# Performance work log

Hardware: AMD Instinct MI355X
Metric: run time of the kernel (lower is better)

Reference implementation:

```python
import jax, jax.numpy as jnp
import numpy as np

NUM_TEAMS = 200000
EMBED_DIM = 16
NUM_EDGES = 3200000
BATCH = 500000
EPS_NORM = 1e-12  # F.normalize clamp
EPS_SOFTMAX = 1e-16  # PyG edge-softmax denom eps
NEG_SLOPE = 0.01  # LeakyReLU default


def setup_inputs() -> dict:
    key = jax.random.key(0)
    ks = jax.random.split(key, 12)
    inp = {}
    inp["embed"] = jax.random.normal(ks[0], (NUM_TEAMS, EMBED_DIM), dtype=jnp.float32)
    inp["beta"] = jnp.ones((2,), dtype=jnp.float32)  # one learnable scalar per AGNNConv
    # torch Linear init ~ U(-1/sqrt(fan_in), 1/sqrt(fan_in)); stored as [in, out]
    def lin(k, fi, fo):
        b = 1.0 / np.sqrt(fi)
        k1, k2 = jax.random.split(k)
        return (jax.random.uniform(k1, (fi, fo), jnp.float32, -b, b),
                jax.random.uniform(k2, (fo,), jnp.float32, -b, b))
    inp["lin0_w"], inp["lin0_b"] = lin(ks[1], 2 * EMBED_DIM, 6)
    inp["lin1_w"], inp["lin1_b"] = lin(ks[2], 6, 16)
    inp["lin2_w"], inp["lin2_b"] = lin(ks[3], 16, 3)
    inp["edge_index"] = jax.random.randint(ks[4], (2, NUM_EDGES), 0, NUM_TEAMS, dtype=jnp.int64)
    inp["home"] = jax.random.randint(ks[5], (BATCH,), 0, NUM_TEAMS, dtype=jnp.int64)
    inp["away"] = jax.random.randint(ks[6], (BATCH,), 0, NUM_TEAMS, dtype=jnp.int64)
    return inp


def _agnn_conv(x, beta, src, dst, n):
    # x: [N, D]; messages flow src(j) -> dst(i); scatter-softmax over edges per dst
    xn = x / jnp.maximum(jnp.linalg.norm(x, axis=-1, keepdims=True), EPS_NORM)
    alpha = beta * jnp.sum(xn[src] * xn[dst], axis=-1)          # [E]
    m = jax.ops.segment_max(alpha, dst, num_segments=n)          # [N]
    a = jnp.exp(alpha - m[dst])                                   # [E]
    denom = jax.ops.segment_sum(a, dst, num_segments=n)          # [N]
    a = a / (denom[dst] + EPS_SOFTMAX)
    return jax.ops.segment_sum(a[:, None] * x[src], dst, num_segments=n)  # [N, D]


def _forward(embed, beta, lin0_w, lin0_b, lin1_w, lin1_b, lin2_w, lin2_b,
             src, dst, home, away):
    n = embed.shape[0]
    act = lambda v: jax.nn.leaky_relu(v, NEG_SLOPE)
    x = embed  # embedding of arange(n_teams) == the table itself
    x = act(_agnn_conv(x, beta[0], src, dst, n))
    x = act(_agnn_conv(x, beta[1], src, dst, n))
    h = jnp.concatenate([x[home], x[away]], axis=-1)  # [B, 2D]
    h = act(h @ lin0_w + lin0_b)
    h = act(h @ lin1_w + lin1_b)
    h = act(h @ lin2_w + lin2_b)
    return jax.nn.log_softmax(h, axis=0).reshape(-1, 3)  # LogSoftmax(dim=0), faithful


def reference(embed, beta, lin0_w, lin0_b, lin1_w, lin1_b, lin2_w, lin2_b,
              edge_index, home, away):
    n = embed.shape[0]
    # AGNNConv default: remove then add self-loops
    loops = jnp.arange(n, dtype=edge_index.dtype)
    mask = edge_index[0] != edge_index[1]
    safe = jnp.where(mask, edge_index[1], edge_index[0])  # self-loop-out non-loop edges
    src = jnp.concatenate([edge_index[0], loops])
    dst = jnp.concatenate([jnp.where(mask, edge_index[1], edge_index[0]), loops])
    # masked self-loops in original list become src==dst duplicates of the appended
    # self-loops only if random collision; to faithfully *remove* them we redirect
    # removed edges onto the node's own appended self-loop (alpha identical for
    # src==dst), which changes only duplicate self-loop counts with prob ~1/N.
    return _forward(embed, beta, lin0_w, lin0_b, lin1_w, lin1_b, lin2_w, lin2_b,
                    src, dst, home, away)
```

## Files before the change

kernel.cpp:

```cpp
#include <hip/hip_runtime.h>
#include <hip/hip_fp16.h>
#include <math.h>

#define TPB 256
#define NPB 512
#define NPB_SHIFT 9
#define EPB 8192
#define EPW 16
#define BCAP 12288
#define RSTRIDE 32

typedef float v2f __attribute__((ext_vector_type(2)));

__device__ __forceinline__ float leaky_relu(float v) { return v > 0.0f ? v : 0.01f * v; }

__device__ __forceinline__ float dot4(float4 a, float4 b) {
    return a.x * b.x + a.y * b.y + a.z * b.z + a.w * b.w;
}
__device__ __forceinline__ float4 f4_scale(float4 a, float s) {
    return make_float4(a.x * s, a.y * s, a.z * s, a.w * s);
}
__device__ __forceinline__ float4 f4_acc(float4 a, float w, float4 y) {
    return make_float4(fmaf(w, y.x, a.x), fmaf(w, y.y, a.y),
                       fmaf(w, y.z, a.z), fmaf(w, y.w, a.w));
}
__device__ __forceinline__ float4 f4_add_shfl(float4 v, int d) {
    return make_float4(v.x + __shfl_xor(v.x, d, 64), v.y + __shfl_xor(v.y, d, 64),
                       v.z + __shfl_xor(v.z, d, 64), v.w + __shfl_xor(v.w, d, 64));
}
__device__ __forceinline__ float4 leaky4(float4 v) {
    return make_float4(leaky_relu(v.x), leaky_relu(v.y), leaky_relu(v.z), leaky_relu(v.w));
}

__device__ __forceinline__ float4 dec4(unsigned w) {
    v2f lo = __builtin_amdgcn_cvt_pk_f32_fp8((int)w, false);
    v2f hi = __builtin_amdgcn_cvt_pk_f32_fp8((int)w, true);
    return make_float4(lo.x, lo.y, hi.x, hi.y);
}
__device__ __forceinline__ unsigned enc4(float4 v) {
    int r = __builtin_amdgcn_cvt_pk_fp8_f32(v.x, v.y, 0, false);
    r = __builtin_amdgcn_cvt_pk_fp8_f32(v.z, v.w, r, true);
    return (unsigned)r;
}

__device__ __forceinline__ void store_h4(__half* row, int l, float4 v) {
    union { float2 f; __half h[4]; } u;
    u.h[0] = __float2half(v.x); u.h[1] = __float2half(v.y);
    u.h[2] = __float2half(v.z); u.h[3] = __float2half(v.w);
    ((float2*)row)[l] = u.f;
}

__device__ __forceinline__ uint4 rec_q(const char* base, int i) {
    return *(const uint4*)(base + (size_t)i * RSTRIDE);
}
__device__ __forceinline__ float rec_n(const char* base, int i) {
    return *(const float*)(base + (size_t)i * RSTRIDE + 16);
}

__device__ __forceinline__ int wave_incl_scan(int v, int lane) {
#pragma unroll
    for (int off = 1; off < 64; off <<= 1) {
        int u = __shfl_up(v, off, 64);
        if (lane >= off) v += u;
    }
    return v;
}

__global__ void k_binA(const int* __restrict__ src, const int* __restrict__ dst,
                       unsigned* __restrict__ bdata, int* __restrict__ cbase,
                       int* __restrict__ ccnt, int E, int K,
                       const float* __restrict__ x, char* __restrict__ xqn,
                       int N) {
    __shared__ int hist[512];
    __shared__ unsigned lcol[EPB];
    __shared__ int wsum[8];
    int t = threadIdx.x;
    int lane = t & 63, wv = t >> 6;
    int c = blockIdx.x;
    int e0 = c * EPB;
    int e1 = min(e0 + EPB, E);
    int tot = e1 - e0;
    hist[t] = 0;
    __syncthreads();
    int myd[EPW], mys[EPW];
    if (tot == EPB) {
        const int4* d4 = (const int4*)(dst + e0);
        const int4* s4 = (const int4*)(src + e0);
#pragma unroll
        for (int k = 0; k < 4; ++k) {
            int4 dd = d4[t + k * 512];
            int4 ss = s4[t + k * 512];
            myd[4 * k + 0] = dd.x; myd[4 * k + 1] = dd.y;
            myd[4 * k + 2] = dd.z; myd[4 * k + 3] = dd.w;
            mys[4 * k + 0] = ss.x; mys[4 * k + 1] = ss.y;
            mys[4 * k + 2] = ss.z; mys[4 * k + 3] = ss.w;
            atomicAdd(&hist[dd.x >> NPB_SHIFT], 1);
            atomicAdd(&hist[dd.y >> NPB_SHIFT], 1);
            atomicAdd(&hist[dd.z >> NPB_SHIFT], 1);
            atomicAdd(&hist[dd.w >> NPB_SHIFT], 1);
        }
    } else {
#pragma unroll
        for (int k = 0; k < EPW; ++k) {
            int e = e0 + t + k * 512;
            int d = (e < e1) ? dst[e] : -1;
            mys[k] = (e < e1) ? src[e] : 0;
            myd[k] = d;
            if (d >= 0) atomicAdd(&hist[d >> NPB_SHIFT], 1);
        }
    }
    __syncthreads();
    int v = hist[t];
    int inc = wave_incl_scan(v, lane);
    if (lane == 63) wsum[wv] = inc;
    __syncthreads();
    if (t == 0) {
        int acc = 0;
#pragma unroll
        for (int k = 0; k < 8; ++k) { int xv = wsum[k]; wsum[k] = acc; acc += xv; }
    }
    __syncthreads();
    int excl = inc + wsum[wv] - v;
    if (t < K) {
        cbase[(size_t)c * K + t] = excl;
        ccnt[(size_t)c * K + t] = v;
    }
    __syncthreads();
    hist[t] = excl;
    __syncthreads();
    if (tot == EPB) {
#pragma unroll
        for (int k = 0; k < EPW; ++k) {
            int d = myd[k];
            int p = atomicAdd(&hist[d >> NPB_SHIFT], 1);
            lcol[p] = ((unsigned)(d & (NPB - 1)) << 18) | (unsigned)mys[k];
        }
    } else {
#pragma unroll
        for (int k = 0; k < EPW; ++k) {
            int d = myd[k];
            if (d >= 0) {
                int p = atomicAdd(&hist[d >> NPB_SHIFT], 1);
                lcol[p] = ((unsigned)(d & (NPB - 1)) << 18) | (unsigned)mys[k];
            }
        }
    }
    __syncthreads();
    unsigned* outp = bdata + (size_t)c * EPB;
    for (int i = t; i < tot; i += 512) outp[i] = lcol[i];
    int i = c * 512 + t;
    if (i < N) {
        const float4* xp = (const float4*)(x + (size_t)i * 16);
        float4 a = xp[0], b = xp[1], cc = xp[2], d = xp[3];
        float ss = dot4(a, a) + dot4(b, b) + dot4(cc, cc) + dot4(d, d);
        float nn = fmaxf(sqrtf(ss), 1e-12f);
        float inv = 1.0f / nn;
        char* rp = xqn + (size_t)i * RSTRIDE;
        *(uint4*)rp = make_uint4(enc4(f4_scale(a, inv)), enc4(f4_scale(b, inv)),
                                 enc4(f4_scale(cc, inv)), enc4(f4_scale(d, inv)));
        *(float*)(rp + 16) = nn;
    }
}

__global__ void k_binB(const unsigned* __restrict__ bdata, const int* __restrict__ cbase,
                       const int* __restrict__ ccnt,
                       int* __restrict__ startp, int* __restrict__ endp,
                       int* __restrict__ col, int N, int NC, int K) {
    __shared__ int cb[512];
    __shared__ int cc[512];
    __shared__ int ldeg[NPB];
    __shared__ int wsum[8];
    int b = blockIdx.x, t = threadIdx.x;
    int lane = t & 63, wv = t >> 6;
    int n0 = b << NPB_SHIFT;
    int nn = min(NPB, N - n0);
    cb[t] = (t < NC) ? cbase[(size_t)t * K + b] : 0;
    cc[t] = (t < NC) ? ccnt[(size_t)t * K + b] : 0;
    ldeg[t] = 0;
    __syncthreads();
    int mycnt = (t < NC) ? cc[t] : 0;
    const unsigned* myp = bdata + (size_t)t * EPB + cb[t];
    for (int k = 0; k < mycnt; ++k) {
        unsigned e = myp[k];
        atomicAdd(&ldeg[e >> 18], 1);
    }
    __syncthreads();
    int dv = ldeg[t];
    int inc = wave_incl_scan(dv, lane);
    if (lane == 63) wsum[wv] = inc;
    __syncthreads();
    if (t == 0) {
        int acc = 0;
#pragma unroll
        for (int k = 0; k < 8; ++k) { int xv = wsum[k]; wsum[k] = acc; acc += xv; }
    }
    __syncthreads();
    int excl = inc + wsum[wv] - dv;
    int gb = b * BCAP;
    if (t < nn) {
        startp[n0 + t] = gb + excl;
        endp[n0 + t] = gb + excl + dv;
    }
    __syncthreads();
    ldeg[t] = excl;
    __syncthreads();
    for (int k = 0; k < mycnt; ++k) {
        unsigned e = myp[k];
        int pos = atomicAdd(&ldeg[e >> 18], 1);
        col[gb + pos] = (int)(e & 0x3FFFFu);
    }
}

__global__ void k_agnn(const char* __restrict__ xqn,
                       const int* __restrict__ startp, const int* __restrict__ endp,
                       const int* __restrict__ col,
                       const float* __restrict__ beta_ptr, int beta_idx,
                       void* __restrict__ out, int n, int fp8_out) {
    int t = threadIdx.x;
    int l = t & 7;
    int i = blockIdx.x * (512 / 8) + (t >> 3);
    if (i >= n) return;
    float bet = beta_ptr[beta_idx];
    uint4 rowi = rec_q(xqn, i);
    float ni = rec_n(xqn, i);
    float4 x0 = dec4(rowi.x), x1 = dec4(rowi.y), x2 = dec4(rowi.z), x3 = dec4(rowi.w);
    float4 q0 = f4_scale(x0, bet), q1 = f4_scale(x1, bet),
           q2 = f4_scale(x2, bet), q3 = f4_scale(x3, bet);
    float s;
    float4 a0, a1, a2, a3;
    if (l == 0) {
        float aself = dot4(x0, q0) + dot4(x1, q1) + dot4(x2, q2) + dot4(x3, q3);
        float w = __expf(aself);
        s = w;
        float wi = w * ni;
        a0 = f4_scale(x0, wi); a1 = f4_scale(x1, wi);
        a2 = f4_scale(x2, wi); a3 = f4_scale(x3, wi);
    } else {
        s = 0.0f;
        a0 = a1 = a2 = a3 = make_float4(0.f, 0.f, 0.f, 0.f);
    }
    int e1 = endp[i];
    int last = max(e1 - 1, 0);
    int e = startp[i] + l;
    int j0 = min(max(col[min(e, last)], 0), n - 1);
    uint4 rA = rec_q(xqn, j0);
    float nA = rec_n(xqn, j0);
    int j1 = min(max(col[min(e + 8, last)], 0), n - 1);
    uint4 rB = rec_q(xqn, j1);
    float nB = rec_n(xqn, j1);
    for (; e < e1; e += 8) {
        int j2 = min(max(col[min(e + 16, last)], 0), n - 1);
        uint4 rC = rec_q(xqn, j2);
        float nC = rec_n(xqn, j2);
        float4 y0 = dec4(rA.x), y1 = dec4(rA.y), y2 = dec4(rA.z), y3 = dec4(rA.w);
        float d = dot4(y0, q0) + dot4(y1, q1) + dot4(y2, q2) + dot4(y3, q3);
        float w = __expf(d);
        s += w;
        float wn = w * nA;
        a0 = f4_acc(a0, wn, y0);
        a1 = f4_acc(a1, wn, y1);
        a2 = f4_acc(a2, wn, y2);
        a3 = f4_acc(a3, wn, y3);
        rA = rB; nA = nB; rB = rC; nB = nC;
    }
#pragma unroll
    for (int d_ = 1; d_ < 8; d_ <<= 1) {
        s += __shfl_xor(s, d_, 64);
        a0 = f4_add_shfl(a0, d_);
        a1 = f4_add_shfl(a1, d_);
        a2 = f4_add_shfl(a2, d_);
        a3 = f4_add_shfl(a3, d_);
    }
    float inv = 1.0f / (s + 1e-16f);
    float4 o0 = leaky4(f4_scale(a0, inv));
    float4 o1 = leaky4(f4_scale(a1, inv));
    float4 o2 = leaky4(f4_scale(a2, inv));
    float4 o3 = leaky4(f4_scale(a3, inv));
    if (l < 4) {
        float4 oq = (l == 0) ? o0 : (l == 1) ? o1 : (l == 2) ? o2 : o3;
        if (fp8_out) {
            float ss = dot4(o0, o0) + dot4(o1, o1) + dot4(o2, o2) + dot4(o3, o3);
            float nn = fmaxf(sqrtf(ss), 1e-12f);
            char* rp = (char*)out + (size_t)i * RSTRIDE;
            ((unsigned*)rp)[l] = enc4(f4_scale(oq, 1.0f / nn));
            if (l == 0) *(float*)(rp + 16) = nn;
        } else {
            store_h4((__half*)out + (size_t)i * 16, l, oq);
        }
    }
}

__global__ void k_mlp(const __half* __restrict__ x, const int* __restrict__ home,
                      const int* __restrict__ away,
                      const float* __restrict__ w0, const float* __restrict__ b0,
                      const float* __restrict__ w1, const float* __restrict__ b1,
                      const float* __restrict__ w2, const float* __restrict__ b2,
                      float* __restrict__ z, float* __restrict__ bmax,
                      float* __restrict__ bsum, int nb) {
    __shared__ float sw0[192], sw1[96], sw2[48], sb0[6], sb1[16], sb2[3];
    __shared__ float rmax[4][3];
    __shared__ float rsum[4][3];
    int t = threadIdx.x;
    if (t < 192) sw0[t] = w0[t];
    if (t < 96)  sw1[t] = w1[t];
    if (t < 48)  sw2[t] = w2[t];
    if (t < 6)   sb0[t] = b0[t];
    if (t < 16)  sb1[t] = b1[t];
    if (t < 3)   sb2[t] = b2[t];
    __syncthreads();
    int i = blockIdx.x * blockDim.x + t;
    bool act = i < nb;
    float z0 = -3.4e38f, z1 = -3.4e38f, z2 = -3.4e38f;
    if (act) {
        float h[32];
        const uint4* hr = (const uint4*)(x + (size_t)home[i] * 16);
        const uint4* ar = (const uint4*)(x + (size_t)away[i] * 16);
        uint4 hv0 = hr[0], hv1 = hr[1];
        uint4 av0 = ar[0], av1 = ar[1];
        union { uint4 u; __half2 h2[4]; } cv;
#pragma unroll
        for (int q = 0; q < 4; ++q) {
            cv.u = (q == 0) ? hv0 : (q == 1) ? hv1 : (q == 2) ? av0 : av1;
#pragma unroll
            for (int k = 0; k < 4; ++k) {
                float2 f = __half22float2(cv.h2[k]);
                h[q * 8 + 2 * k + 0] = f.x;
                h[q * 8 + 2 * k + 1] = f.y;
            }
        }
        float t0[6];
#pragma unroll
        for (int o = 0; o < 6; ++o) {
            float acc = sb0[o];
#pragma unroll
            for (int k = 0; k < 32; ++k) acc = fmaf(h[k], sw0[k * 6 + o], acc);
            t0[o] = leaky_relu(acc);
        }
        float t1[16];
#pragma unroll
        for (int o = 0; o < 16; ++o) {
            float acc = sb1[o];
#pragma unroll
            for (int k = 0; k < 6; ++k) acc = fmaf(t0[k], sw1[k * 16 + o], acc);
            t1[o] = leaky_relu(acc);
        }
        float zz[3];
#pragma unroll
        for (int o = 0; o < 3; ++o) {
            float acc = sb2[o];
#pragma unroll
            for (int k = 0; k < 16; ++k) acc = fmaf(t1[k], sw2[k * 3 + o], acc);
            zz[o] = leaky_relu(acc);
            z[(size_t)i * 3 + o] = zz[o];
        }
        z0 = zz[0]; z1 = zz[1]; z2 = zz[2];
    }
    float w0_ = z0, w1_ = z1, w2_ = z2;
#pragma unroll
    for (int off = 32; off > 0; off >>= 1) {
        w0_ = fmaxf(w0_, __shfl_down(w0_, off));
        w1_ = fmaxf(w1_, __shfl_down(w1_, off));
        w2_ = fmaxf(w2_, __shfl_down(w2_, off));
    }
    int wid = t >> 6;
    if ((t & 63) == 0) { rmax[wid][0] = w0_; rmax[wid][1] = w1_; rmax[wid][2] = w2_; }
    __syncthreads();
    float M0 = fmaxf(fmaxf(rmax[0][0], rmax[1][0]), fmaxf(rmax[2][0], rmax[3][0]));
    float M1 = fmaxf(fmaxf(rmax[0][1], rmax[1][1]), fmaxf(rmax[2][1], rmax[3][1]));
    float M2 = fmaxf(fmaxf(rmax[0][2], rmax[1][2]), fmaxf(rmax[2][2], rmax[3][2]));
    float e0 = act ? __expf(z0 - M0) : 0.0f;
    float e1 = act ? __expf(z1 - M1) : 0.0f;
    float e2 = act ? __expf(z2 - M2) : 0.0f;
#pragma unroll
    for (int off = 32; off > 0; off >>= 1) {
        e0 += __shfl_down(e0, off);
        e1 += __shfl_down(e1, off);
        e2 += __shfl_down(e2, off);
    }
    if ((t & 63) == 0) { rsum[wid][0] = e0; rsum[wid][1] = e1; rsum[wid][2] = e2; }
    __syncthreads();
    if (t == 0) {
        float S0 = rsum[0][0] + rsum[1][0] + rsum[2][0] + rsum[3][0];
        float S1 = rsum[0][1] + rsum[1][1] + rsum[2][1] + rsum[3][1];
        float S2 = rsum[0][2] + rsum[1][2] + rsum[2][2] + rsum[3][2];
        bmax[blockIdx.x * 3 + 0] = M0; bmax[blockIdx.x * 3 + 1] = M1; bmax[blockIdx.x * 3 + 2] = M2;
        bsum[blockIdx.x * 3 + 0] = S0; bsum[blockIdx.x * 3 + 1] = S1; bsum[blockIdx.x * 3 + 2] = S2;
    }
}

__global__ void k_lse(const float* __restrict__ bmax, const float* __restrict__ bsum,
                      float* __restrict__ gM, float* __restrict__ gS, int nblk) {
    __shared__ float lm[4][3];
    __shared__ float ls[4][3];
    int t = threadIdx.x;
    float M0 = -3.4e38f, M1 = -3.4e38f, M2 = -3.4e38f;
    float S0 = 0.f, S1 = 0.f, S2 = 0.f;
    for (int b = t; b < nblk; b += 256) {
        float m0 = bmax[b * 3 + 0], s0 = bsum[b * 3 + 0];
        float n0 = fmaxf(M0, m0); S0 = S0 * __expf(M0 - n0) + s0 * __expf(m0 - n0); M0 = n0;
        float m1 = bmax[b * 3 + 1], s1 = bsum[b * 3 + 1];
        float n1 = fmaxf(M1, m1); S1 = S1 * __expf(M1 - n1) + s1 * __expf(m1 - n1); M1 = n1;
        float m2 = bmax[b * 3 + 2], s2 = bsum[b * 3 + 2];
        float n2 = fmaxf(M2, m2); S2 = S2 * __expf(M2 - n2) + s2 * __expf(m2 - n2); M2 = n2;
    }
#pragma unroll
    for (int off = 32; off > 0; off >>= 1) {
        float mo, so, nm;
        mo = __shfl_down(M0, off); so = __shfl_down(S0, off);
        nm = fmaxf(M0, mo); S0 = S0 * __expf(M0 - nm) + so * __expf(mo - nm); M0 = nm;
        mo = __shfl_down(M1, off); so = __shfl_down(S1, off);
        nm = fmaxf(M1, mo); S1 = S1 * __expf(M1 - nm) + so * __expf(mo - nm); M1 = nm;
        mo = __shfl_down(M2, off); so = __shfl_down(S2, off);
        nm = fmaxf(M2, mo); S2 = S2 * __expf(M2 - nm) + so * __expf(mo - nm); M2 = nm;
    }
    int wid = t >> 6;
    if ((t & 63) == 0) {
        lm[wid][0] = M0; lm[wid][1] = M1; lm[wid][2] = M2;
        ls[wid][0] = S0; ls[wid][1] = S1; ls[wid][2] = S2;
    }
    __syncthreads();
    if (t == 0) {
        for (int w = 1; w < 4; ++w) {
            float nm;
            nm = fmaxf(M0, lm[w][0]); S0 = S0 * __expf(M0 - nm) + ls[w][0] * __expf(lm[w][0] - nm); M0 = nm;
            nm = fmaxf(M1, lm[w][1]); S1 = S1 * __expf(M1 - nm) + ls[w][1] * __expf(lm[w][1] - nm); M1 = nm;
            nm = fmaxf(M2, lm[w][2]); S2 = S2 * __expf(M2 - nm) + ls[w][2] * __expf(lm[w][2] - nm); M2 = nm;
        }
        gM[0] = M0; gM[1] = M1; gM[2] = M2;
        gS[0] = S0; gS[1] = S1; gS[2] = S2;
    }
}

__device__ __forceinline__ float pick3(int c, float L0, float L1, float L2) {
    return c == 0 ? L0 : (c == 1 ? L1 : L2);
}

__global__ void k_final(const float4* __restrict__ z4, const float* __restrict__ gM,
                        const float* __restrict__ gS, float4* __restrict__ out4, int n4) {
    int i = blockIdx.x * blockDim.x + threadIdx.x;
    if (i >= n4) return;
    float L0 = gM[0] + logf(gS[0]);
    float L1 = gM[1] + logf(gS[1]);
    float L2 = gM[2] + logf(gS[2]);
    float4 v = z4[i];
    int c = i % 3;
    int c1 = (c + 1) % 3, c2 = (c + 2) % 3;
    out4[i] = make_float4(v.x - pick3(c, L0, L1, L2),
                          v.y - pick3(c1, L0, L1, L2),
                          v.z - pick3(c2, L0, L1, L2),
                          v.w - pick3(c, L0, L1, L2));
}

extern "C" void kernel_launch(void* const* d_in, const int* in_sizes, int n_in,
                              void* d_out, int out_size, void* d_ws, size_t ws_size,
                              hipStream_t stream) {
    const float* embed = (const float*)d_in[0];
    const float* beta  = (const float*)d_in[1];
    const float* w0 = (const float*)d_in[2];
    const float* b0 = (const float*)d_in[3];
    const float* w1 = (const float*)d_in[4];
    const float* b1 = (const float*)d_in[5];
    const float* w2 = (const float*)d_in[6];
    const float* b2 = (const float*)d_in[7];
    const int* eidx = (const int*)d_in[8];
    const int* home = (const int*)d_in[9];
    const int* away = (const int*)d_in[10];

    const int N = in_sizes[0] / 16;
    const int E = in_sizes[8] / 2;
    const int B = in_sizes[9];
    const int* esrc = eidx;
    const int* edst = eidx + E;
    const int K = (N + NPB - 1) >> NPB_SHIFT;
    const int NC = (E + EPB - 1) / EPB;

    char* ws = (char*)d_ws;
    size_t off = 0;
    auto alloc = [&](size_t bytes) -> char* {
        off = (off + 255) & ~(size_t)255;
        char* p = ws + off;
        off += bytes;
        return p;
    };
    size_t bdata_bytes = (size_t)NC * EPB * 4;
    size_t alias_bytes = (((size_t)N * RSTRIDE + 511) & ~(size_t)255) + (size_t)B * 3 * 4;
    char* U = alloc(bdata_bytes > alias_bytes ? bdata_bytes : alias_bytes);
    unsigned* bdata = (unsigned*)U;
    char* xqn1  = U;
    float* zbuf = (float*)(U + (((size_t)N * RSTRIDE + 511) & ~(size_t)255));

    int* startp  = (int*)alloc((size_t)N * 4);
    int* endp    = (int*)alloc((size_t)N * 4);
    int* colw    = (int*)alloc((size_t)K * BCAP * 4);
    int* cbase   = (int*)alloc((size_t)NC * K * 4);
    int* ccnt    = (int*)alloc((size_t)NC * K * 4);
    char* xqn0   = alloc((size_t)N * RSTRIDE);
    __half* xh2  = (__half*)alloc((size_t)N * 32);
    const int nblkB = (B + TPB - 1) / TPB;
    float* bmax  = (float*)alloc((size_t)nblkB * 3 * 4);
    float* bsum  = (float*)alloc((size_t)nblkB * 3 * 4);
    float* gM    = (float*)alloc(16);
    float* gS    = (float*)alloc(16);
    (void)ws_size; (void)n_in; (void)out_size;

    k_binA<<<NC, 512, 0, stream>>>(esrc, edst, bdata, cbase, ccnt, E, K,
                                   embed, xqn0, N);
    k_binB<<<K, 512, 0, stream>>>(bdata, cbase, ccnt, startp, endp, colw, N, NC, K);

    const int nblkN8 = (N + 63) / 64;
    k_agnn<<<nblkN8, 512, 0, stream>>>(xqn0, startp, endp, colw, beta, 0, xqn1, N, 1);
    k_agnn<<<nblkN8, 512, 0, stream>>>(xqn1, startp, endp, colw, beta, 1, xh2, N, 0);

    k_mlp<<<nblkB, TPB, 0, stream>>>(xh2, home, away, w0, b0, w1, b1, w2, b2,
                                     zbuf, bmax, bsum, B);
    k_lse<<<1, 256, 0, stream>>>(bmax, bsum, gM, gS, nblkB);
    const int n4 = (B * 3) / 4;
    k_final<<<(n4 + TPB - 1) / TPB, TPB, 0, stream>>>((const float4*)zbuf, gM, gS,
                                                      (float4*)d_out, n4);
}
```

Baseline: 234.5 us.

## Pack edge ranges, predicate neighbor prefetch, fold LSE reduction into final kernel

Start/end offsets are packed into one int2 array so each node needs a single load. The neighbor prefetch is now predicated instead of clamping indices, which avoids redundant gathers for short adjacency lists. The self-loop score is replaced by exp(beta), relying on the normalized row having unit norm, which drops one 16-wide dot product per node. The separate single-block log-sum-exp kernel is removed and every final block recomputes the global reduction from the per-block partials, saving a launch at the cost of redundant reduction work in each block.

Result: slower. 240.5 us (+2.6%).

```diff
diff --git a/kernel.cpp b/kernel.cpp
--- a/kernel.cpp
+++ b/kernel.cpp
@@ -164,7 +164,7 @@
 
 __global__ void k_binB(const unsigned* __restrict__ bdata, const int* __restrict__ cbase,
                        const int* __restrict__ ccnt,
-                       int* __restrict__ startp, int* __restrict__ endp,
+                       int2* __restrict__ rng,
                        int* __restrict__ col, int N, int NC, int K) {
     __shared__ int cb[512];
     __shared__ int cc[512];
@@ -198,8 +198,7 @@
     int excl = inc + wsum[wv] - dv;
     int gb = b * BCAP;
     if (t < nn) {
-        startp[n0 + t] = gb + excl;
-        endp[n0 + t] = gb + excl + dv;
+        rng[n0 + t] = make_int2(gb + excl, gb + excl + dv);
     }
     __syncthreads();
     ldeg[t] = excl;
@@ -212,7 +211,7 @@
 }
 
 __global__ void k_agnn(const char* __restrict__ xqn,
-                       const int* __restrict__ startp, const int* __restrict__ endp,
+                       const int2* __restrict__ rng,
                        const int* __restrict__ col,
                        const float* __restrict__ beta_ptr, int beta_idx,
                        void* __restrict__ out, int n, int fp8_out) {
@@ -229,8 +228,7 @@
     float s;
     float4 a0, a1, a2, a3;
     if (l == 0) {
-        float aself = dot4(x0, q0) + dot4(x1, q1) + dot4(x2, q2) + dot4(x3, q3);
-        float w = __expf(aself);
+        float w = __expf(bet);
         s = w;
         float wi = w * ni;
         a0 = f4_scale(x0, wi); a1 = f4_scale(x1, wi);
@@ -239,19 +237,26 @@
         s = 0.0f;
         a0 = a1 = a2 = a3 = make_float4(0.f, 0.f, 0.f, 0.f);
     }
-    int e1 = endp[i];
-    int last = max(e1 - 1, 0);
-    int e = startp[i] + l;
-    int j0 = min(max(col[min(e, last)], 0), n - 1);
-    uint4 rA = rec_q(xqn, j0);
-    float nA = rec_n(xqn, j0);
-    int j1 = min(max(col[min(e + 8, last)], 0), n - 1);
-    uint4 rB = rec_q(xqn, j1);
-    float nB = rec_n(xqn, j1);
+    int2 se = rng[i];
+    int e1 = se.y;
+    int e = se.x + l;
+    uint4 rA = make_uint4(0u, 0u, 0u, 0u), rB = make_uint4(0u, 0u, 0u, 0u);
+    float nA = 0.0f, nB = 0.0f;
+    if (e < e1) {
+        int j = col[e];
+        rA = rec_q(xqn, j); nA = rec_n(xqn, j);
+    }
+    if (e + 8 < e1) {
+        int j = col[e + 8];
+        rB = rec_q(xqn, j); nB = rec_n(xqn, j);
+    }
     for (; e < e1; e += 8) {
-        int j2 = min(max(col[min(e + 16, last)], 0), n - 1);
-        uint4 rC = rec_q(xqn, j2);
-        float nC = rec_n(xqn, j2);
+        uint4 rC = make_uint4(0u, 0u, 0u, 0u);
+        float nC = 0.0f;
+        if (e + 16 < e1) {
+            int j = col[e + 16];
+            rC = rec_q(xqn, j); nC = rec_n(xqn, j);
+        }
         float4 y0 = dec4(rA.x), y1 = dec4(rA.y), y2 = dec4(rA.z), y3 = dec4(rA.w);
         float d = dot4(y0, q0) + dot4(y1, q1) + dot4(y2, q2) + dot4(y3, q3);
         float w = __expf(d);
@@ -388,10 +393,16 @@
     }
 }
 
-__global__ void k_lse(const float* __restrict__ bmax, const float* __restrict__ bsum,
-                      float* __restrict__ gM, float* __restrict__ gS, int nblk) {
+__device__ __forceinline__ float pick3(int c, float L0, float L1, float L2) {
+    return c == 0 ? L0 : (c == 1 ? L1 : L2);
+}
+
+__global__ void k_final(const float4* __restrict__ z4,
+                        const float* __restrict__ bmax, const float* __restrict__ bsum,
+                        int nblk, float4* __restrict__ out4, int n4) {
     __shared__ float lm[4][3];
     __shared__ float ls[4][3];
+    __shared__ float Lsh[3];
     int t = threadIdx.x;
     float M0 = -3.4e38f, M1 = -3.4e38f, M2 = -3.4e38f;
     float S0 = 0.f, S1 = 0.f, S2 = 0.f;
@@ -426,22 +437,14 @@
             nm = fmaxf(M1, lm[w][1]); S1 = S1 * __expf(M1 - nm) + ls[w][1] * __expf(lm[w][1] - nm); M1 = nm;
             nm = fmaxf(M2, lm[w][2]); S2 = S2 * __expf(M2 - nm) + ls[w][2] * __expf(lm[w][2] - nm); M2 = nm;
         }
-        gM[0] = M0; gM[1] = M1; gM[2] = M2;
-        gS[0] = S0; gS[1] = S1; gS[2] = S2;
-    }
-}
-
-__device__ __forceinline__ float pick3(int c, float L0, float L1, float L2) {
-    return c == 0 ? L0 : (c == 1 ? L1 : L2);
-}
-
-__global__ void k_final(const float4* __restrict__ z4, const float* __restrict__ gM,
-                        const float* __restrict__ gS, float4* __restrict__ out4, int n4) {
-    int i = blockIdx.x * blockDim.x + threadIdx.x;
+        Lsh[0] = M0 + logf(S0);
+        Lsh[1] = M1 + logf(S1);
+        Lsh[2] = M2 + logf(S2);
+    }
+    __syncthreads();
+    float L0 = Lsh[0], L1 = Lsh[1], L2 = Lsh[2];
+    int i = blockIdx.x * blockDim.x + t;
     if (i >= n4) return;
-    float L0 = gM[0] + logf(gS[0]);
-    float L1 = gM[1] + logf(gS[1]);
-    float L2 = gM[2] + logf(gS[2]);
     float4 v = z4[i];
     int c = i % 3;
     int c1 = (c + 1) % 3, c2 = (c + 2) % 3;
@@ -489,8 +492,7 @@
     char* xqn1  = U;
     float* zbuf = (float*)(U + (((size_t)N * RSTRIDE + 511) & ~(size_t)255));
 
-    int* startp  = (int*)alloc((size_t)N * 4);
-    int* endp    = (int*)alloc((size_t)N * 4);
+    int2* rng    = (int2*)alloc((size_t)N * 8);
     int* colw    = (int*)alloc((size_t)K * BCAP * 4);
     int* cbase   = (int*)alloc((size_t)NC * K * 4);
     int* ccnt    = (int*)alloc((size_t)NC * K * 4);
@@ -499,22 +501,19 @@
     const int nblkB = (B + TPB - 1) / TPB;
     float* bmax  = (float*)alloc((size_t)nblkB * 3 * 4);
     float* bsum  = (float*)alloc((size_t)nblkB * 3 * 4);
-    float* gM    = (float*)alloc(16);
-    float* gS    = (float*)alloc(16);
     (void)ws_size; (void)n_in; (void)out_size;
 
     k_binA<<<NC, 512, 0, stream>>>(esrc, edst, bdata, cbase, ccnt, E, K,
                                    embed, xqn0, N);
-    k_binB<<<K, 512, 0, stream>>>(bdata, cbase, ccnt, startp, endp, colw, N, NC, K);
+    k_binB<<<K, 512, 0, stream>>>(bdata, cbase, ccnt, rng, colw, N, NC, K);
 
     const int nblkN8 = (N + 63) / 64;
-    k_agnn<<<nblkN8, 512, 0, stream>>>(xqn0, startp, endp, colw, beta, 0, xqn1, N, 1);
-    k_agnn<<<nblkN8, 512, 0, stream>>>(xqn1, startp, endp, colw, beta, 1, xh2, N, 0);
+    k_agnn<<<nblkN8, 512, 0, stream>>>(xqn0, rng, colw, beta, 0, xqn1, N, 1);
+    k_agnn<<<nblkN8, 512, 0, stream>>>(xqn1, rng, colw, beta, 1, xh2, N, 0);
 
     k_mlp<<<nblkB, TPB, 0, stream>>>(xh2, home, away, w0, b0, w1, b1, w2, b2,
                                      zbuf, bmax, bsum, B);
-    k_lse<<<1, 256, 0, stream>>>(bmax, bsum, gM, gS, nblkB);
     const int n4 = (B * 3) / 4;
-    k_final<<<(n4 + TPB - 1) / TPB, TPB, 0, stream>>>((const float4*)zbuf, gM, gS,
-                                                      (float4*)d_out, n4);
-}
+    k_final<<<(n4 + TPB - 1) / TPB, TPB, 0, stream>>>((const float4*)zbuf, bmax, bsum,
+                                                      nblkB, (float4*)d_out, n4);
+}
```
